# Optimization experiments

Hardware: AMD Instinct MI355X
Metric: run time of the kernel (lower is better)

## Reference

```python
import jax, jax.numpy as jnp
import numpy as np

TARGET_FRAMES = 16
VOXEL_LAMBDA = 20.0
CONF_THRESHOLD = 0.1
CONF_PERCENTILE = 50.0
G = 48  # per-axis voxel grid cap (lambda=20 => ~20-40 occupied cells/axis for randn points)


def setup_inputs() -> dict:
    key = jax.random.key(0)
    k1, k2, k3, k4, k5 = jax.random.split(key, 5)
    B, S, H, W = 1, 128, 224, 224
    return {
        "depth": jax.random.uniform(k1, (B, S, H, W, 1), dtype=jnp.float32),
        "depth_conf": jax.random.uniform(k2, (B, S, H, W), dtype=jnp.float32),
        "world_points": jax.random.normal(k3, (B, S, H, W, 3), dtype=jnp.float32),
        "world_points_conf": jax.random.uniform(k4, (B, S, H, W), dtype=jnp.float32),
        "pose_enc": jax.random.normal(k5, (B, S, 9), dtype=jnp.float32),
    }


def _voxel_occupancy(world_points, world_points_conf):
    # world_points: [1,S,H,W,3], conf: [1,S,H,W]
    pts = world_points[0].reshape(world_points.shape[1], -1, 3)   # [S, HW, 3]
    conf = world_points_conf[0].reshape(world_points.shape[1], -1)  # [S, HW]
    # per-frame confidence filter: conf > thr AND conf >= per-frame percentile
    pct = jnp.quantile(conf, CONF_PERCENTILE / 100.0, axis=1)       # [S]
    valid = (conf > CONF_THRESHOLD) & (conf >= pct[:, None])        # [S, HW]
    big = jnp.float32(1e30)
    pmin = jnp.min(jnp.where(valid[..., None], pts, big), axis=(0, 1))   # [3]
    pmax = jnp.max(jnp.where(valid[..., None], pts, -big), axis=(0, 1))  # [3]
    voxel_size = jnp.min(pmax - pmin) / VOXEL_LAMBDA  # adaptive voxel size
    idx = jnp.floor((pts - pmin) / voxel_size).astype(jnp.int32)
    idx = jnp.clip(idx, 0, G - 1)
    vid = (idx[..., 0] * G + idx[..., 1]) * G + idx[..., 2]  # [S, HW]
    V = G * G * G
    vid = jnp.where(valid, vid, V)  # invalid points -> trash bin V
    S = pts.shape[0]
    occ = jnp.zeros((S, V + 1), dtype=bool).at[jnp.arange(S)[:, None], vid].set(True)
    return occ[:, :V]  # [S, V] per-frame voxel occupancy bitmaps


def _greedy_max_coverage(occ, k):
    S, V = occ.shape

    def step(carry, _):
        covered, selected = carry  # [V] bool, [S] bool
        gains = jnp.sum(occ & ~covered[None, :], axis=1).astype(jnp.float32)  # [S]
        gains = jnp.where(selected, -1.0, gains)
        best = jnp.argmax(gains)  # first max == greedy in-order tie-break
        covered = covered | occ[best]
        selected = selected.at[best].set(True)
        return (covered, selected), (best.astype(jnp.int32), gains[best])

    (covered, _), (sel, scores) = jax.lax.scan(
        step, (jnp.zeros((V,), bool), jnp.zeros((S,), bool)), None, length=k)
    return sel, scores, covered


def reference(depth, depth_conf, world_points, world_points_conf, pose_enc):
    occ = _voxel_occupancy(world_points, world_points_conf)
    sel, scores, covered = _greedy_max_coverage(occ, TARGET_FRAMES)
    total_coverage = jnp.sum(covered).astype(jnp.int32)
    # selected_indices [1,K], coverage_scores [1,K], total_coverage scalar
    return sel[None, :], scores[None, :], total_coverage
```

## Files before the change

### kernel.cpp

```cpp
#include <hip/hip_runtime.h>
#include <hip/hip_bf16.h>
#include <cstdint>

#define S_FRAMES 128
#define HW       50176
#define NGRP     12544
#define GDIM     48
#define VWORDS   3456
#define NBINS    4096
#define CAP      512
#define KSEL     16

#define UWC      512u
#define UCAP_BITS 16384u
#define RQ       9

#define OCCA_OFF  0u
#define OCCB_OFF  (128u*3456u)
#define MM_OFF    (2u*128u*3456u)
#define PCT_OFF   (MM_OFF + 64u*16u)
#define FLAG_OFF  (PCT_OFF + 128u)
#define UW_OFF    (FLAG_OFF + 1u)
#define UNI_OFF   (FLAG_OFF + 16u)
#define CMP_OFF   (UNI_OFF + VWORDS)
#define VB_OFF    (CMP_OFF + 128u*UWC)
#define ZR1_N     1024u
#define ZR2_N     (16u + VWORDS)
#define ZR_TOT    (ZR1_N + ZR2_N)

__device__ __forceinline__ unsigned fkey(float f) {
    unsigned u = __float_as_uint(f);
    return (u & 0x80000000u) ? ~u : (u | 0x80000000u);
}
__device__ __forceinline__ float funkey(unsigned k) {
    unsigned u = (k & 0x80000000u) ? (k & 0x7fffffffu) : ~k;
    return __uint_as_float(u);
}

__global__ __launch_bounds__(1024) void pct_kernel(const float* __restrict__ conf,
                                                   float* __restrict__ pct,
                                                   unsigned* __restrict__ ws) {
    const int s = blockIdx.x;
    const int tid = threadIdx.x;
    const int lane = tid & 63, wid = tid >> 6;
    const float4* c4 = (const float4*)(conf + (size_t)s * HW);

    if (tid < 36) {
        unsigned idx = (unsigned)s * 36u + tid;
        if (idx < ZR_TOT) {
            if (idx < ZR1_N) ws[MM_OFF + idx] = 0u;
            else             ws[FLAG_OFF + (idx - ZR1_N)] = 0u;
        }
    }

    __shared__ unsigned hist[NBINS];
    __shared__ unsigned wtot[16];
    __shared__ unsigned woff[16];
    __shared__ float    list[CAP];
    __shared__ unsigned cnt;
    __shared__ int      rbin[2];
    __shared__ unsigned rcum[2];
    __shared__ float    ab[2];

    for (int b = tid; b < NBINS; b += 1024) hist[b] = 0;
    if (tid == 0) cnt = 0;
    __syncthreads();

    for (int g = tid; g < NGRP; g += 1024) {
        float4 v = c4[g];
        int b0 = min(max((int)(v.x * 4096.0f), 0), NBINS - 1);
        int b1 = min(max((int)(v.y * 4096.0f), 0), NBINS - 1);
        int b2 = min(max((int)(v.z * 4096.0f), 0), NBINS - 1);
        int b3 = min(max((int)(v.w * 4096.0f), 0), NBINS - 1);
        atomicAdd(&hist[b0], 1u); atomicAdd(&hist[b1], 1u);
        atomicAdd(&hist[b2], 1u); atomicAdd(&hist[b3], 1u);
    }
    __syncthreads();

    unsigned chunk = hist[tid * 4] + hist[tid * 4 + 1] + hist[tid * 4 + 2] + hist[tid * 4 + 3];
    unsigned x = chunk;
#pragma unroll
    for (int m = 1; m < 64; m <<= 1) {
        unsigned y = (unsigned)__shfl_up((int)x, m);
        if (lane >= m) x += y;
    }
    if (lane == 63) wtot[wid] = x;
    __syncthreads();
    if (tid < 16) {
        unsigned acc = 0;
        for (int w = 0; w < tid; w++) acc += wtot[w];
        woff[tid] = acc;
    }
    __syncthreads();
    unsigned excl = x - chunk + woff[wid];

    const unsigned R0 = 25087u, R1 = 25088u;
#pragma unroll
    for (int r = 0; r < 2; r++) {
        unsigned rr = r ? R1 : R0;
        if (rr >= excl && rr < excl + chunk) {
            unsigned cum = excl;
            for (int j = 0; j < 4; j++) {
                unsigned h = hist[tid * 4 + j];
                if (rr < cum + h) { rbin[r] = tid * 4 + j; rcum[r] = cum; break; }
                cum += h;
            }
        }
    }
    __syncthreads();

    const int blo = rbin[0], bhi = rbin[1];
    const unsigned cumLo = rcum[0];

    for (int g = tid; g < NGRP; g += 1024) {
        float4 v = c4[g];
        float vv[4] = {v.x, v.y, v.z, v.w};
#pragma unroll
        for (int j = 0; j < 4; j++) {
            int b = min(max((int)(vv[j] * 4096.0f), 0), NBINS - 1);
            if (b >= blo && b <= bhi) {
                unsigned pos = atomicAdd(&cnt, 1u);
                if (pos < CAP) list[pos] = vv[j];
            }
        }
    }
    __syncthreads();

    const int n = (int)min(cnt, (unsigned)CAP);
    const int r0 = (int)(R0 - cumLo), r1 = (int)(R1 - cumLo);
    for (int e = tid; e < n; e += 1024) {
        float xx = list[e];
        int rank = 0;
        for (int j = 0; j < n; j++) {
            float y = list[j];
            rank += (y < xx) || (y == xx && j < e);
        }
        if (rank == r0) ab[0] = xx;
        if (rank == r1) ab[1] = xx;
    }
    __syncthreads();
    if (tid == 0) pct[s] = 0.5f * ab[0] + 0.5f * ab[1];
}

__global__ __launch_bounds__(256) void minmax_kernel(const float* __restrict__ wp,
                                                     const float* __restrict__ conf,
                                                     const float* __restrict__ pct,
                                                     unsigned* __restrict__ ws) {
    const int s = blockIdx.y;
    const int tid = threadIdx.x;
    const int gidx = blockIdx.x * 256 + tid;
    const float pc = pct[s];
    const size_t base = (size_t)s * HW;

    const float4 cf = ((const float4*)(conf + base))[gidx];
    const float4* wp4 = (const float4*)(wp + base * 3) + (size_t)gidx * 3;
    const float4 a = wp4[0], b = wp4[1], d = wp4[2];

    const float BIG = 3.402823466e38f;
    float mnx = BIG, mny = BIG, mnz = BIG;
    float mxx = -BIG, mxy = -BIG, mxz = -BIG;

    float px[4] = {a.x, a.w, b.z, d.y};
    float py[4] = {a.y, b.x, b.w, d.z};
    float pz[4] = {a.z, b.y, d.x, d.w};
    float cc[4] = {cf.x, cf.y, cf.z, cf.w};
    unsigned nib = 0;
#pragma unroll
    for (int j = 0; j < 4; j++) {
        bool v = (cc[j] > 0.1f) && (cc[j] >= pc);
        nib |= (v ? 1u : 0u) << j;
        float x = v ? px[j] : BIG, y = v ? py[j] : BIG, z = v ? pz[j] : BIG;
        mnx = fminf(mnx, x); mny = fminf(mny, y); mnz = fminf(mnz, z);
        x = v ? px[j] : -BIG; y = v ? py[j] : -BIG; z = v ? pz[j] : -BIG;
        mxx = fmaxf(mxx, x); mxy = fmaxf(mxy, y); mxz = fmaxf(mxz, z);
    }

    __shared__ unsigned vbw[32];
    if (tid < 32) vbw[tid] = 0;
    __syncthreads();
    if (nib) atomicOr(&vbw[tid >> 3], nib << ((tid & 7) * 4));

#pragma unroll
    for (int m = 32; m >= 1; m >>= 1) {
        mnx = fminf(mnx, __shfl_xor(mnx, m)); mny = fminf(mny, __shfl_xor(mny, m));
        mnz = fminf(mnz, __shfl_xor(mnz, m));
        mxx = fmaxf(mxx, __shfl_xor(mxx, m)); mxy = fmaxf(mxy, __shfl_xor(mxy, m));
        mxz = fmaxf(mxz, __shfl_xor(mxz, m));
    }
    __shared__ float red[4][6];
    if ((tid & 63) == 0) {
        int w = tid >> 6;
        red[w][0] = mnx; red[w][1] = mny; red[w][2] = mnz;
        red[w][3] = mxx; red[w][4] = mxy; red[w][5] = mxz;
    }
    __syncthreads();
    if (tid < 32)
        ws[VB_OFF + (unsigned)s * 1568u + (unsigned)blockIdx.x * 32u + tid] = vbw[tid];
    if (tid == 0) {
        float r0 = red[0][0], r1 = red[0][1], r2 = red[0][2];
        float r3 = red[0][3], r4 = red[0][4], r5 = red[0][5];
        for (int w = 1; w < 4; w++) {
            r0 = fminf(r0, red[w][0]); r1 = fminf(r1, red[w][1]); r2 = fminf(r2, red[w][2]);
            r3 = fmaxf(r3, red[w][3]); r4 = fmaxf(r4, red[w][4]); r5 = fmaxf(r5, red[w][5]);
        }
        unsigned* slot = ws + MM_OFF + (unsigned)((blockIdx.x + blockIdx.y * 49) & 63) * 16;
        atomicMax(slot + 0, fkey(-r0));
        atomicMax(slot + 1, fkey(-r1));
        atomicMax(slot + 2, fkey(-r2));
        atomicMax(slot + 3, fkey(r3));
        atomicMax(slot + 4, fkey(r4));
        atomicMax(slot + 5, fkey(r5));
    }
}

__global__ __launch_bounds__(512) void voxel_kernel(const float* __restrict__ wp,
                                                    unsigned* __restrict__ ws) {
    const int s = blockIdx.x >> 1;
    const int part = blockIdx.x & 1;
    const int tid = threadIdx.x;

    __shared__ unsigned bm[VWORDS];
    __shared__ float prm[4];
    for (int w = tid; w < VWORDS; w += 512) bm[w] = 0;

    if (tid < 64) {
        const unsigned* sl = ws + MM_OFF + (unsigned)tid * 16;
        unsigned k0 = sl[0], k1 = sl[1], k2 = sl[2], k3 = sl[3], k4 = sl[4], k5 = sl[5];
#pragma unroll
        for (int m = 32; m >= 1; m >>= 1) {
            k0 = max(k0, (unsigned)__shfl_xor((int)k0, m));
            k1 = max(k1, (unsigned)__shfl_xor((int)k1, m));
            k2 = max(k2, (unsigned)__shfl_xor((int)k2, m));
            k3 = max(k3, (unsigned)__shfl_xor((int)k3, m));
            k4 = max(k4, (unsigned)__shfl_xor((int)k4, m));
            k5 = max(k5, (unsigned)__shfl_xor((int)k5, m));
        }
        if (tid == 0) {
            float p0 = -funkey(k0), p1 = -funkey(k1), p2 = -funkey(k2);
            float d0 = funkey(k3) - p0, d1 = funkey(k4) - p1, d2 = funkey(k5) - p2;
            prm[0] = p0; prm[1] = p1; prm[2] = p2;
            prm[3] = fminf(d0, fminf(d1, d2)) / 20.0f;
        }
    }
    __syncthreads();

    const float pmx = prm[0], pmy = prm[1], pmz = prm[2], vs = prm[3];
    const size_t base = (size_t)s * HW;
    const float4* w4 = (const float4*)(wp + base * 3);
    const unsigned* vb = ws + VB_OFF + (unsigned)s * 1568u;

#pragma unroll 1
    for (int k = 0; k < 13; k++) {
        int gl = k * 512 + tid;
        if (gl >= 6272) break;
        int g = part * 6272 + gl;
        unsigned nib = (vb[g >> 3] >> ((g & 7) * 4)) & 0xFu;
        if (!nib) continue;
        const float4* wg = w4 + (size_t)g * 3;
        float4 a = wg[0], b = wg[1], d = wg[2];
        float px[4] = {a.x, a.w, b.z, d.y};
        float py[4] = {a.y, b.x, b.w, d.z};
        float pz[4] = {a.z, b.y, d.x, d.w};
#pragma unroll
        for (int j = 0; j < 4; j++) {
            if ((nib >> j) & 1u) {
                int ix = min(max((int)floorf((px[j] - pmx) / vs), 0), GDIM - 1);
                int iy = min(max((int)floorf((py[j] - pmy) / vs), 0), GDIM - 1);
                int iz = min(max((int)floorf((pz[j] - pmz) / vs), 0), GDIM - 1);
                int vid = (ix * GDIM + iy) * GDIM + iz;
                atomicOr(&bm[vid >> 5], 1u << (vid & 31));
            }
        }
    }
    __syncthreads();

    unsigned* occ = ws + (part ? OCCB_OFF : OCCA_OFF) + (unsigned)s * VWORDS;
    for (int w = tid; w < VWORDS; w += 512) {
        unsigned v = bm[w];
        occ[w] = v;
        if (v) atomicOr(&ws[UNI_OFF + w], v);
    }
}

__global__ __launch_bounds__(1024) void remap_kernel(unsigned* __restrict__ ws) {
    const int f = blockIdx.x;
    const int tid = threadIdx.x;
    const int lane = tid & 63, wid = tid >> 6;

    __shared__ unsigned uni[VWORDS];
    __shared__ unsigned short basew[VWORDS];
    __shared__ unsigned cbm[UWC];
    __shared__ unsigned wtot[16];
    __shared__ unsigned woff[16];
    __shared__ unsigned Ush;

    for (int w = tid; w < VWORDS; w += 1024) uni[w] = ws[UNI_OFF + w];
    for (int w = tid; w < (int)UWC; w += 1024) cbm[w] = 0;
    __syncthreads();

    const int w0 = tid * 4;
    unsigned chunk = 0;
#pragma unroll
    for (int j = 0; j < 4; j++) { int w = w0 + j; if (w < VWORDS) chunk += __popc(uni[w]); }
    unsigned x = chunk;
#pragma unroll
    for (int m = 1; m < 64; m <<= 1) {
        unsigned y = (unsigned)__shfl_up((int)x, m);
        if (lane >= m) x += y;
    }
    if (lane == 63) wtot[wid] = x;
    __syncthreads();
    if (tid < 16) {
        unsigned acc = 0;
        for (int w = 0; w < tid; w++) acc += wtot[w];
        woff[tid] = acc;
    }
    __syncthreads();
    unsigned running = x - chunk + woff[wid];
#pragma unroll
    for (int j = 0; j < 4; j++) {
        int w = w0 + j;
        if (w < VWORDS) { basew[w] = (unsigned short)running; running += __popc(uni[w]); }
    }
    if (tid == 1023) Ush = running;
    __syncthreads();
    const unsigned U = Ush;
    if (f == 0 && tid == 0) { ws[FLAG_OFF] = (U <= UCAP_BITS) ? 2u : 1u; ws[UW_OFF] = (U + 31) >> 5; }
    if (U > UCAP_BITS) return;

    const unsigned* pA = ws + OCCA_OFF + (unsigned)f * VWORDS;
    const unsigned* pB = ws + OCCB_OFF + (unsigned)f * VWORDS;
    for (int w = tid; w < VWORDS; w += 1024) {
        unsigned v = pA[w] | pB[w];
        if (!v) continue;
        unsigned uw = uni[w], b0 = basew[w];
        while (v) {
            int b = __ffs(v) - 1; v &= v - 1;
            unsigned cid = b0 + (unsigned)__popc(uw & ((1u << b) - 1u));
            atomicOr(&cbm[cid >> 5], 1u << (cid & 31));
        }
    }
    __syncthreads();
    for (int w = tid; w < (int)UWC; w += 1024) ws[CMP_OFF + (unsigned)f * UWC + w] = cbm[w];
}

__global__ __launch_bounds__(1024, 1) void greedy1_kernel(unsigned* __restrict__ ws,
                                                          float* __restrict__ out) {
    if (ws[FLAG_OFF] != 2u) return;
    const int tid = threadIdx.x;
    const int f = tid >> 3, sl = tid & 7;
    const unsigned UW = ws[UW_OFF];

    __shared__ unsigned cov[UWC];
    __shared__ int gains[S_FRAMES];
    __shared__ unsigned bestsh;

    for (int w = tid; w < (int)UWC; w += 1024) cov[w] = 0u;
    bool selF = false;
    int best = -1;

    if (UW <= 32u * RQ) {
        uint4 occw[RQ];
        const uint4* my4 = (const uint4*)(ws + CMP_OFF + (unsigned)f * UWC) + sl * RQ;
#pragma unroll
        for (int j = 0; j < RQ; j++) occw[j] = my4[j];
        __syncthreads();

        for (int it = 0; it < KSEL; it++) {
            if (best >= 0 && f == best) {
#pragma unroll
                for (int j = 0; j < RQ; j++) {
                    int w = (sl * RQ + j) * 4;
                    cov[w] |= occw[j].x; cov[w + 1] |= occw[j].y;
                    cov[w + 2] |= occw[j].z; cov[w + 3] |= occw[j].w;
                }
            }
            __syncthreads();
            int g = 0;
#pragma unroll
            for (int j = 0; j < RQ; j++) {
                int w = (sl * RQ + j) * 4;
                g += __popc(occw[j].x & ~cov[w]) + __popc(occw[j].y & ~cov[w + 1])
                   + __popc(occw[j].z & ~cov[w + 2]) + __popc(occw[j].w & ~cov[w + 3]);
            }
            g += __shfl_xor(g, 1); g += __shfl_xor(g, 2); g += __shfl_xor(g, 4);
            if (sl == 0) gains[f] = selF ? -1 : g;
            __syncthreads();
            if (tid < 64) {
                int g1 = gains[tid], g2 = gains[tid + 64];
                unsigned k1 = (g1 < 0) ? 0u : (((unsigned)g1 << 7) | (unsigned)(127 - tid));
                unsigned k2 = (g2 < 0) ? 0u : (((unsigned)g2 << 7) | (unsigned)(63 - tid));
                unsigned k = max(k1, k2);
#pragma unroll
                for (int m = 32; m >= 1; m >>= 1) k = max(k, (unsigned)__shfl_xor((int)k, m));
                if (tid == 0) {
                    bestsh = k;
                    out[it] = (float)(127 - (int)(k & 127u));
                    out[KSEL + it] = (float)(k >> 7);
                }
            }
            __syncthreads();
            best = 127 - (int)(bestsh & 127u);
            if (f == best) selF = true;
        }
        if (f == best) {
#pragma unroll
            for (int j = 0; j < RQ; j++) {
                int w = (sl * RQ + j) * 4;
                cov[w] |= occw[j].x; cov[w + 1] |= occw[j].y;
                cov[w + 2] |= occw[j].z; cov[w + 3] |= occw[j].w;
            }
        }
        __syncthreads();
        if (f == 0) {
            int t = 0;
#pragma unroll
            for (int j = 0; j < RQ; j++) {
                int w = (sl * RQ + j) * 4;
                t += __popc(cov[w]) + __popc(cov[w + 1]) + __popc(cov[w + 2]) + __popc(cov[w + 3]);
            }
            t += __shfl_xor(t, 1); t += __shfl_xor(t, 2); t += __shfl_xor(t, 4);
            if (sl == 0) out[2 * KSEL] = (float)t;
        }
    } else {
        const int Q = (int)((UW + 31) >> 5);
        const uint4* my4 = (const uint4*)(ws + CMP_OFF + (unsigned)f * UWC) + sl * Q;
        __syncthreads();

        for (int it = 0; it < KSEL; it++) {
            if (best >= 0 && f == best) {
                const uint4* b4 = (const uint4*)(ws + CMP_OFF + (unsigned)best * UWC) + sl * Q;
#pragma unroll 4
                for (int j = 0; j < Q; j++) {
                    uint4 o = b4[j];
                    int w = (sl * Q + j) * 4;
                    cov[w] |= o.x; cov[w + 1] |= o.y; cov[w + 2] |= o.z; cov[w + 3] |= o.w;
                }
            }
            __syncthreads();
            int g = 0;
#pragma unroll 4
            for (int j = 0; j < Q; j++) {
                uint4 o = my4[j];
                int w = (sl * Q + j) * 4;
                g += __popc(o.x & ~cov[w]) + __popc(o.y & ~cov[w + 1])
                   + __popc(o.z & ~cov[w + 2]) + __popc(o.w & ~cov[w + 3]);
            }
            g += __shfl_xor(g, 1); g += __shfl_xor(g, 2); g += __shfl_xor(g, 4);
            if (sl == 0) gains[f] = selF ? -1 : g;
            __syncthreads();
            if (tid < 64) {
                int g1 = gains[tid], g2 = gains[tid + 64];
                unsigned k1 = (g1 < 0) ? 0u : (((unsigned)g1 << 7) | (unsigned)(127 - tid));
                unsigned k2 = (g2 < 0) ? 0u : (((unsigned)g2 << 7) | (unsigned)(63 - tid));
                unsigned k = max(k1, k2);
#pragma unroll
                for (int m = 32; m >= 1; m >>= 1) k = max(k, (unsigned)__shfl_xor((int)k, m));
                if (tid == 0) {
                    bestsh = k;
                    out[it] = (float)(127 - (int)(k & 127u));
                    out[KSEL + it] = (float)(k >> 7);
                }
            }
            __syncthreads();
            best = 127 - (int)(bestsh & 127u);
            if (f == best) selF = true;
        }
        if (f == best) {
            const uint4* b4 = (const uint4*)(ws + CMP_OFF + (unsigned)best * UWC) + sl * Q;
#pragma unroll 4
            for (int j = 0; j < Q; j++) {
                uint4 o = b4[j];
                int w = (sl * Q + j) * 4;
                cov[w] |= o.x; cov[w + 1] |= o.y; cov[w + 2] |= o.z; cov[w + 3] |= o.w;
            }
        }
        __syncthreads();
        if (f == 0) {
            int t = 0;
#pragma unroll 4
            for (int j = 0; j < Q; j++) {
                int w = (sl * Q + j) * 4;
                t += __popc(cov[w]) + __popc(cov[w + 1]) + __popc(cov[w + 2]) + __popc(cov[w + 3]);
            }
            t += __shfl_xor(t, 1); t += __shfl_xor(t, 2); t += __shfl_xor(t, 4);
            if (sl == 0) out[2 * KSEL] = (float)t;
        }
    }
}

extern "C" void kernel_launch(void* const* d_in, const int* in_sizes, int n_in,
                              void* d_out, int out_size, void* d_ws, size_t ws_size,
                              hipStream_t stream) {
    const float* wp   = (const float*)d_in[2];
    const float* conf = (const float*)d_in[3];
    float* out = (float*)d_out;
    unsigned* ws = (unsigned*)d_ws;

    float* pct = (float*)(ws + PCT_OFF);
    pct_kernel<<<128, 1024, 0, stream>>>(conf, pct, ws);
    minmax_kernel<<<dim3(49, 128), 256, 0, stream>>>(wp, conf, pct, ws);
    voxel_kernel<<<256, 512, 0, stream>>>(wp, ws);
    remap_kernel<<<128, 1024, 0, stream>>>(ws);
    greedy1_kernel<<<1, 1024, 0, stream>>>(ws, out);
}
```

Before: 229.0 us.

## Fuse percentile with min/max pass and greedy into remap via last-block counter

Merges the percentile and min/max kernels, so each frame's block computes its median and then scans only valid points for bounds and validity bits. It stores per-frame min/max directly instead of using atomic sortable keys. The greedy selection now runs in the last remap block, chosen through an atomic ticket counter, which cuts launches from five to three. The trade-off is much less parallelism in the min/max pass (128 blocks instead of 6272) and a threadfence-based handoff between blocks.

```diff
diff --git a/kernel.cpp b/kernel.cpp
--- a/kernel.cpp
+++ b/kernel.cpp
@@ -10,6 +10,7 @@
 #define NBINS    4096
 #define CAP      512
 #define KSEL     16
+#define VBW      1568
 
 #define UWC      512u
 #define UCAP_BITS 16384u
@@ -18,42 +19,24 @@
 #define OCCA_OFF  0u
 #define OCCB_OFF  (128u*3456u)
 #define MM_OFF    (2u*128u*3456u)
-#define PCT_OFF   (MM_OFF + 64u*16u)
-#define FLAG_OFF  (PCT_OFF + 128u)
-#define UW_OFF    (FLAG_OFF + 1u)
-#define UNI_OFF   (FLAG_OFF + 16u)
+#define CTR_OFF   (MM_OFF + 1024u)
+#define UNI_OFF   (CTR_OFF + 16u)
 #define CMP_OFF   (UNI_OFF + VWORDS)
 #define VB_OFF    (CMP_OFF + 128u*UWC)
-#define ZR1_N     1024u
-#define ZR2_N     (16u + VWORDS)
-#define ZR_TOT    (ZR1_N + ZR2_N)
-
-__device__ __forceinline__ unsigned fkey(float f) {
-    unsigned u = __float_as_uint(f);
-    return (u & 0x80000000u) ? ~u : (u | 0x80000000u);
-}
-__device__ __forceinline__ float funkey(unsigned k) {
-    unsigned u = (k & 0x80000000u) ? (k & 0x7fffffffu) : ~k;
-    return __uint_as_float(u);
-}
-
-__global__ __launch_bounds__(1024) void pct_kernel(const float* __restrict__ conf,
-                                                   float* __restrict__ pct,
-                                                   unsigned* __restrict__ ws) {
+
+__global__ __launch_bounds__(1024) void fused_stats_kernel(const float* __restrict__ conf,
+                                                           const float* __restrict__ wp,
+                                                           unsigned* __restrict__ ws) {
     const int s = blockIdx.x;
     const int tid = threadIdx.x;
     const int lane = tid & 63, wid = tid >> 6;
     const float4* c4 = (const float4*)(conf + (size_t)s * HW);
 
-    if (tid < 36) {
-        unsigned idx = (unsigned)s * 36u + tid;
-        if (idx < ZR_TOT) {
-            if (idx < ZR1_N) ws[MM_OFF + idx] = 0u;
-            else             ws[FLAG_OFF + (idx - ZR1_N)] = 0u;
-        }
-    }
+    if (tid < 27) ws[UNI_OFF + (unsigned)s * 27u + tid] = 0u;
+    if (s == 0 && tid == 31) ws[CTR_OFF] = 0u;
 
     __shared__ unsigned hist[NBINS];
+    __shared__ unsigned vbw[VBW];
     __shared__ unsigned wtot[16];
     __shared__ unsigned woff[16];
     __shared__ float    list[CAP];
@@ -61,8 +44,11 @@
     __shared__ int      rbin[2];
     __shared__ unsigned rcum[2];
     __shared__ float    ab[2];
+    __shared__ float    medsh;
+    __shared__ float    red[16][6];
 
     for (int b = tid; b < NBINS; b += 1024) hist[b] = 0;
+    for (int w = tid; w < VBW; w += 1024) vbw[w] = 0;
     if (tid == 0) cnt = 0;
     __syncthreads();
 
@@ -139,46 +125,41 @@
         if (rank == r1) ab[1] = xx;
     }
     __syncthreads();
-    if (tid == 0) pct[s] = 0.5f * ab[0] + 0.5f * ab[1];
-}
-
-__global__ __launch_bounds__(256) void minmax_kernel(const float* __restrict__ wp,
-                                                     const float* __restrict__ conf,
-                                                     const float* __restrict__ pct,
-                                                     unsigned* __restrict__ ws) {
-    const int s = blockIdx.y;
-    const int tid = threadIdx.x;
-    const int gidx = blockIdx.x * 256 + tid;
-    const float pc = pct[s];
+    if (tid == 0) medsh = 0.5f * ab[0] + 0.5f * ab[1];
+    __syncthreads();
+    const float med = medsh;
+
     const size_t base = (size_t)s * HW;
-
-    const float4 cf = ((const float4*)(conf + base))[gidx];
-    const float4* wp4 = (const float4*)(wp + base * 3) + (size_t)gidx * 3;
-    const float4 a = wp4[0], b = wp4[1], d = wp4[2];
-
+    const float4* wp4 = (const float4*)(wp + base * 3);
     const float BIG = 3.402823466e38f;
     float mnx = BIG, mny = BIG, mnz = BIG;
     float mxx = -BIG, mxy = -BIG, mxz = -BIG;
 
-    float px[4] = {a.x, a.w, b.z, d.y};
-    float py[4] = {a.y, b.x, b.w, d.z};
-    float pz[4] = {a.z, b.y, d.x, d.w};
-    float cc[4] = {cf.x, cf.y, cf.z, cf.w};
-    unsigned nib = 0;
-#pragma unroll
-    for (int j = 0; j < 4; j++) {
-        bool v = (cc[j] > 0.1f) && (cc[j] >= pc);
-        nib |= (v ? 1u : 0u) << j;
-        float x = v ? px[j] : BIG, y = v ? py[j] : BIG, z = v ? pz[j] : BIG;
-        mnx = fminf(mnx, x); mny = fminf(mny, y); mnz = fminf(mnz, z);
-        x = v ? px[j] : -BIG; y = v ? py[j] : -BIG; z = v ? pz[j] : -BIG;
-        mxx = fmaxf(mxx, x); mxy = fmaxf(mxy, y); mxz = fmaxf(mxz, z);
-    }
-
-    __shared__ unsigned vbw[32];
-    if (tid < 32) vbw[tid] = 0;
-    __syncthreads();
-    if (nib) atomicOr(&vbw[tid >> 3], nib << ((tid & 7) * 4));
+    for (int g = tid; g < NGRP; g += 1024) {
+        float4 v = c4[g];
+        float cc[4] = {v.x, v.y, v.z, v.w};
+        unsigned nib = 0;
+#pragma unroll
+        for (int j = 0; j < 4; j++) {
+            bool val = (cc[j] > 0.1f) && (cc[j] >= med);
+            nib |= (val ? 1u : 0u) << j;
+        }
+        if (nib) {
+            atomicOr(&vbw[g >> 3], nib << ((g & 7) * 4));
+            const float4* wg = wp4 + (size_t)g * 3;
+            float4 a = wg[0], bb = wg[1], d = wg[2];
+            float px[4] = {a.x, a.w, bb.z, d.y};
+            float py[4] = {a.y, bb.x, bb.w, d.z};
+            float pz[4] = {a.z, bb.y, d.x, d.w};
+#pragma unroll
+            for (int j = 0; j < 4; j++) {
+                if ((nib >> j) & 1u) {
+                    mnx = fminf(mnx, px[j]); mny = fminf(mny, py[j]); mnz = fminf(mnz, pz[j]);
+                    mxx = fmaxf(mxx, px[j]); mxy = fmaxf(mxy, py[j]); mxz = fmaxf(mxz, pz[j]);
+                }
+            }
+        }
+    }
 
 #pragma unroll
     for (int m = 32; m >= 1; m >>= 1) {
@@ -187,59 +168,50 @@
         mxx = fmaxf(mxx, __shfl_xor(mxx, m)); mxy = fmaxf(mxy, __shfl_xor(mxy, m));
         mxz = fmaxf(mxz, __shfl_xor(mxz, m));
     }
-    __shared__ float red[4][6];
-    if ((tid & 63) == 0) {
-        int w = tid >> 6;
-        red[w][0] = mnx; red[w][1] = mny; red[w][2] = mnz;
-        red[w][3] = mxx; red[w][4] = mxy; red[w][5] = mxz;
-    }
-    __syncthreads();
-    if (tid < 32)
-        ws[VB_OFF + (unsigned)s * 1568u + (unsigned)blockIdx.x * 32u + tid] = vbw[tid];
+    if (lane == 0) {
+        red[wid][0] = mnx; red[wid][1] = mny; red[wid][2] = mnz;
+        red[wid][3] = mxx; red[wid][4] = mxy; red[wid][5] = mxz;
+    }
+    __syncthreads();
     if (tid == 0) {
-        float r0 = red[0][0], r1 = red[0][1], r2 = red[0][2];
-        float r3 = red[0][3], r4 = red[0][4], r5 = red[0][5];
-        for (int w = 1; w < 4; w++) {
-            r0 = fminf(r0, red[w][0]); r1 = fminf(r1, red[w][1]); r2 = fminf(r2, red[w][2]);
-            r3 = fmaxf(r3, red[w][3]); r4 = fmaxf(r4, red[w][4]); r5 = fmaxf(r5, red[w][5]);
-        }
-        unsigned* slot = ws + MM_OFF + (unsigned)((blockIdx.x + blockIdx.y * 49) & 63) * 16;
-        atomicMax(slot + 0, fkey(-r0));
-        atomicMax(slot + 1, fkey(-r1));
-        atomicMax(slot + 2, fkey(-r2));
-        atomicMax(slot + 3, fkey(r3));
-        atomicMax(slot + 4, fkey(r4));
-        atomicMax(slot + 5, fkey(r5));
-    }
+        float r0f = red[0][0], r1f = red[0][1], r2f = red[0][2];
+        float r3f = red[0][3], r4f = red[0][4], r5f = red[0][5];
+        for (int w = 1; w < 16; w++) {
+            r0f = fminf(r0f, red[w][0]); r1f = fminf(r1f, red[w][1]); r2f = fminf(r2f, red[w][2]);
+            r3f = fmaxf(r3f, red[w][3]); r4f = fmaxf(r4f, red[w][4]); r5f = fmaxf(r5f, red[w][5]);
+        }
+        float* slot = (float*)(ws + MM_OFF) + (size_t)s * 8;
+        slot[0] = r0f; slot[1] = r1f; slot[2] = r2f;
+        slot[3] = r3f; slot[4] = r4f; slot[5] = r5f;
+    }
+    for (int w = tid; w < VBW; w += 1024) ws[VB_OFF + (unsigned)s * 1568u + w] = vbw[w];
 }
 
-__global__ __launch_bounds__(512) void voxel_kernel(const float* __restrict__ wp,
-                                                    unsigned* __restrict__ ws) {
+__global__ __launch_bounds__(1024) void voxel_kernel(const float* __restrict__ wp,
+                                                     unsigned* __restrict__ ws) {
     const int s = blockIdx.x >> 1;
     const int part = blockIdx.x & 1;
     const int tid = threadIdx.x;
 
     __shared__ unsigned bm[VWORDS];
     __shared__ float prm[4];
-    for (int w = tid; w < VWORDS; w += 512) bm[w] = 0;
+    for (int w = tid; w < VWORDS; w += 1024) bm[w] = 0;
 
     if (tid < 64) {
-        const unsigned* sl = ws + MM_OFF + (unsigned)tid * 16;
-        unsigned k0 = sl[0], k1 = sl[1], k2 = sl[2], k3 = sl[3], k4 = sl[4], k5 = sl[5];
+        const float* m0 = (const float*)(ws + MM_OFF) + (size_t)tid * 8;
+        const float* m1 = m0 + 64 * 8;
+        float mnx = fminf(m0[0], m1[0]), mny = fminf(m0[1], m1[1]), mnz = fminf(m0[2], m1[2]);
+        float mxx = fmaxf(m0[3], m1[3]), mxy = fmaxf(m0[4], m1[4]), mxz = fmaxf(m0[5], m1[5]);
 #pragma unroll
         for (int m = 32; m >= 1; m >>= 1) {
-            k0 = max(k0, (unsigned)__shfl_xor((int)k0, m));
-            k1 = max(k1, (unsigned)__shfl_xor((int)k1, m));
-            k2 = max(k2, (unsigned)__shfl_xor((int)k2, m));
-            k3 = max(k3, (unsigned)__shfl_xor((int)k3, m));
-            k4 = max(k4, (unsigned)__shfl_xor((int)k4, m));
-            k5 = max(k5, (unsigned)__shfl_xor((int)k5, m));
+            mnx = fminf(mnx, __shfl_xor(mnx, m)); mny = fminf(mny, __shfl_xor(mny, m));
+            mnz = fminf(mnz, __shfl_xor(mnz, m));
+            mxx = fmaxf(mxx, __shfl_xor(mxx, m)); mxy = fmaxf(mxy, __shfl_xor(mxy, m));
+            mxz = fmaxf(mxz, __shfl_xor(mxz, m));
         }
         if (tid == 0) {
-            float p0 = -funkey(k0), p1 = -funkey(k1), p2 = -funkey(k2);
-            float d0 = funkey(k3) - p0, d1 = funkey(k4) - p1, d2 = funkey(k5) - p2;
-            prm[0] = p0; prm[1] = p1; prm[2] = p2;
-            prm[3] = fminf(d0, fminf(d1, d2)) / 20.0f;
+            prm[0] = mnx; prm[1] = mny; prm[2] = mnz;
+            prm[3] = fminf(mxx - mnx, fminf(mxy - mny, mxz - mnz)) / 20.0f;
         }
     }
     __syncthreads();
@@ -250,8 +222,8 @@
     const unsigned* vb = ws + VB_OFF + (unsigned)s * 1568u;
 
 #pragma unroll 1
-    for (int k = 0; k < 13; k++) {
-        int gl = k * 512 + tid;
+    for (int k = 0; k < 7; k++) {
+        int gl = k * 1024 + tid;
         if (gl >= 6272) break;
         int g = part * 6272 + gl;
         unsigned nib = (vb[g >> 3] >> ((g & 7) * 4)) & 0xFu;
@@ -275,14 +247,15 @@
     __syncthreads();
 
     unsigned* occ = ws + (part ? OCCB_OFF : OCCA_OFF) + (unsigned)s * VWORDS;
-    for (int w = tid; w < VWORDS; w += 512) {
+    for (int w = tid; w < VWORDS; w += 1024) {
         unsigned v = bm[w];
         occ[w] = v;
         if (v) atomicOr(&ws[UNI_OFF + w], v);
     }
 }
 
-__global__ __launch_bounds__(1024) void remap_kernel(unsigned* __restrict__ ws) {
+__global__ __launch_bounds__(1024, 1) void remap_greedy_kernel(unsigned* __restrict__ ws,
+                                                               float* __restrict__ out) {
     const int f = blockIdx.x;
     const int tid = threadIdx.x;
     const int lane = tid & 63, wid = tid >> 6;
@@ -293,6 +266,10 @@
     __shared__ unsigned wtot[16];
     __shared__ unsigned woff[16];
     __shared__ unsigned Ush;
+    __shared__ unsigned rank_sh;
+    __shared__ unsigned cov[UWC];
+    __shared__ int gains[S_FRAMES];
+    __shared__ unsigned bestsh;
 
     for (int w = tid; w < VWORDS; w += 1024) uni[w] = ws[UNI_OFF + w];
     for (int w = tid; w < (int)UWC; w += 1024) cbm[w] = 0;
@@ -325,7 +302,6 @@
     if (tid == 1023) Ush = running;
     __syncthreads();
     const unsigned U = Ush;
-    if (f == 0 && tid == 0) { ws[FLAG_OFF] = (U <= UCAP_BITS) ? 2u : 1u; ws[UW_OFF] = (U + 31) >> 5; }
     if (U > UCAP_BITS) return;
 
     const unsigned* pA = ws + OCCA_OFF + (unsigned)f * VWORDS;
@@ -342,18 +318,18 @@
     }
     __syncthreads();
     for (int w = tid; w < (int)UWC; w += 1024) ws[CMP_OFF + (unsigned)f * UWC + w] = cbm[w];
-}
-
-__global__ __launch_bounds__(1024, 1) void greedy1_kernel(unsigned* __restrict__ ws,
-                                                          float* __restrict__ out) {
-    if (ws[FLAG_OFF] != 2u) return;
-    const int tid = threadIdx.x;
-    const int f = tid >> 3, sl = tid & 7;
-    const unsigned UW = ws[UW_OFF];
-
-    __shared__ unsigned cov[UWC];
-    __shared__ int gains[S_FRAMES];
-    __shared__ unsigned bestsh;
+
+    __syncthreads();
+    if (tid == 0) {
+        __threadfence();
+        rank_sh = atomicAdd(&ws[CTR_OFF], 1u);
+    }
+    __syncthreads();
+    if (rank_sh != (unsigned)(S_FRAMES - 1)) return;
+    __threadfence();
+
+    const int gf = tid >> 3, sl = tid & 7;
+    const unsigned UW = (U + 31u) >> 5;
 
     for (int w = tid; w < (int)UWC; w += 1024) cov[w] = 0u;
     bool selF = false;
@@ -361,13 +337,13 @@
 
     if (UW <= 32u * RQ) {
         uint4 occw[RQ];
-        const uint4* my4 = (const uint4*)(ws + CMP_OFF + (unsigned)f * UWC) + sl * RQ;
+        const uint4* my4 = (const uint4*)(ws + CMP_OFF + (unsigned)gf * UWC) + sl * RQ;
 #pragma unroll
         for (int j = 0; j < RQ; j++) occw[j] = my4[j];
         __syncthreads();
 
         for (int it = 0; it < KSEL; it++) {
-            if (best >= 0 && f == best) {
+            if (best >= 0 && gf == best) {
 #pragma unroll
                 for (int j = 0; j < RQ; j++) {
                     int w = (sl * RQ + j) * 4;
@@ -384,7 +360,7 @@
                    + __popc(occw[j].z & ~cov[w + 2]) + __popc(occw[j].w & ~cov[w + 3]);
             }
             g += __shfl_xor(g, 1); g += __shfl_xor(g, 2); g += __shfl_xor(g, 4);
-            if (sl == 0) gains[f] = selF ? -1 : g;
+            if (sl == 0) gains[gf] = selF ? -1 : g;
             __syncthreads();
             if (tid < 64) {
                 int g1 = gains[tid], g2 = gains[tid + 64];
@@ -401,9 +377,9 @@
             }
             __syncthreads();
             best = 127 - (int)(bestsh & 127u);
-            if (f == best) selF = true;
-        }
-        if (f == best) {
+            if (gf == best) selF = true;
+        }
+        if (gf == best) {
 #pragma unroll
             for (int j = 0; j < RQ; j++) {
                 int w = (sl * RQ + j) * 4;
@@ -412,7 +388,7 @@
             }
         }
         __syncthreads();
-        if (f == 0) {
+        if (gf == 0) {
             int t = 0;
 #pragma unroll
             for (int j = 0; j < RQ; j++) {
@@ -424,11 +400,11 @@
         }
     } else {
         const int Q = (int)((UW + 31) >> 5);
-        const uint4* my4 = (const uint4*)(ws + CMP_OFF + (unsigned)f * UWC) + sl * Q;
+        const uint4* my4 = (const uint4*)(ws + CMP_OFF + (unsigned)gf * UWC) + sl * Q;
         __syncthreads();
 
         for (int it = 0; it < KSEL; it++) {
-            if (best >= 0 && f == best) {
+            if (best >= 0 && gf == best) {
                 const uint4* b4 = (const uint4*)(ws + CMP_OFF + (unsigned)best * UWC) + sl * Q;
 #pragma unroll 4
                 for (int j = 0; j < Q; j++) {
@@ -447,7 +423,7 @@
                    + __popc(o.z & ~cov[w + 2]) + __popc(o.w & ~cov[w + 3]);
             }
             g += __shfl_xor(g, 1); g += __shfl_xor(g, 2); g += __shfl_xor(g, 4);
-            if (sl == 0) gains[f] = selF ? -1 : g;
+            if (sl == 0) gains[gf] = selF ? -1 : g;
             __syncthreads();
             if (tid < 64) {
                 int g1 = gains[tid], g2 = gains[tid + 64];
@@ -464,9 +440,9 @@
             }
             __syncthreads();
             best = 127 - (int)(bestsh & 127u);
-            if (f == best) selF = true;
-        }
-        if (f == best) {
+            if (gf == best) selF = true;
+        }
+        if (gf == best) {
             const uint4* b4 = (const uint4*)(ws + CMP_OFF + (unsigned)best * UWC) + sl * Q;
 #pragma unroll 4
             for (int j = 0; j < Q; j++) {
@@ -476,7 +452,7 @@
             }
         }
         __syncthreads();
-        if (f == 0) {
+        if (gf == 0) {
             int t = 0;
 #pragma unroll 4
             for (int j = 0; j < Q; j++) {
@@ -497,10 +473,7 @@
     float* out = (float*)d_out;
     unsigned* ws = (unsigned*)d_ws;
 
-    float* pct = (float*)(ws + PCT_OFF);
-    pct_kernel<<<128, 1024, 0, stream>>>(conf, pct, ws);
-    minmax_kernel<<<dim3(49, 128), 256, 0, stream>>>(wp, conf, pct, ws);
-    voxel_kernel<<<256, 512, 0, stream>>>(wp, ws);
-    remap_kernel<<<128, 1024, 0, stream>>>(ws);
-    greedy1_kernel<<<1, 1024, 0, stream>>>(ws, out);
+    fused_stats_kernel<<<128, 1024, 0, stream>>>(conf, wp, ws);
+    voxel_kernel<<<256, 1024, 0, stream>>>(wp, ws);
+    remap_greedy_kernel<<<128, 1024, 0, stream>>>(ws, out);
 }
```

Result: slower. 235.4 us (+2.8%).

## Split histogram across two blocks per frame and fuse remap with greedy via last-block

Applied to the files above, without the earlier changes.

Each frame's confidence histogram is now built by two blocks that merge into a global histogram, and whichever block arrives last computes the median. Remap and greedy selection are merged into one kernel, with the last finishing block running the greedy step, which removes a launch and the flag handshake. The voxel kernel moves to 1024 threads and issues its point loads before the validity check. Workspace zeroing moves to a hipMemsetAsync that now also clears the 128x4096 global histogram, adding memory traffic and an extra stream op.

```diff
diff --git a/kernel.cpp b/kernel.cpp
--- a/kernel.cpp
+++ b/kernel.cpp
@@ -5,11 +5,13 @@
 #define S_FRAMES 128
 #define HW       50176
 #define NGRP     12544
+#define HALFG    6272
 #define GDIM     48
 #define VWORDS   3456
 #define NBINS    4096
 #define CAP      512
 #define KSEL     16
+#define VBW      1568
 
 #define UWC      512u
 #define UCAP_BITS 16384u
@@ -18,15 +20,14 @@
 #define OCCA_OFF  0u
 #define OCCB_OFF  (128u*3456u)
 #define MM_OFF    (2u*128u*3456u)
-#define PCT_OFF   (MM_OFF + 64u*16u)
-#define FLAG_OFF  (PCT_OFF + 128u)
-#define UW_OFF    (FLAG_OFF + 1u)
-#define UNI_OFF   (FLAG_OFF + 16u)
-#define CMP_OFF   (UNI_OFF + VWORDS)
+#define CTR_OFF   (MM_OFF + 1024u)
+#define HCTR_OFF  (CTR_OFF + 16u)
+#define UNI_OFF   (HCTR_OFF + 128u)
+#define HIST_OFF  (UNI_OFF + VWORDS)
+#define ZERO_WORDS (1024u + 16u + 128u + VWORDS + 128u*4096u)
+#define PCT_OFF   (HIST_OFF + 128u*4096u)
+#define CMP_OFF   (PCT_OFF + 128u)
 #define VB_OFF    (CMP_OFF + 128u*UWC)
-#define ZR1_N     1024u
-#define ZR2_N     (16u + VWORDS)
-#define ZR_TOT    (ZR1_N + ZR2_N)
 
 __device__ __forceinline__ unsigned fkey(float f) {
     unsigned u = __float_as_uint(f);
@@ -37,21 +38,14 @@
     return __uint_as_float(u);
 }
 
-__global__ __launch_bounds__(1024) void pct_kernel(const float* __restrict__ conf,
-                                                   float* __restrict__ pct,
-                                                   unsigned* __restrict__ ws) {
-    const int s = blockIdx.x;
+__global__ __launch_bounds__(1024) void hist_median_kernel(const float* __restrict__ conf,
+                                                           float* __restrict__ pct,
+                                                           unsigned* __restrict__ ws) {
+    const int s = blockIdx.x >> 1;
+    const int half = blockIdx.x & 1;
     const int tid = threadIdx.x;
     const int lane = tid & 63, wid = tid >> 6;
     const float4* c4 = (const float4*)(conf + (size_t)s * HW);
-
-    if (tid < 36) {
-        unsigned idx = (unsigned)s * 36u + tid;
-        if (idx < ZR_TOT) {
-            if (idx < ZR1_N) ws[MM_OFF + idx] = 0u;
-            else             ws[FLAG_OFF + (idx - ZR1_N)] = 0u;
-        }
-    }
 
     __shared__ unsigned hist[NBINS];
     __shared__ unsigned wtot[16];
@@ -61,13 +55,14 @@
     __shared__ int      rbin[2];
     __shared__ unsigned rcum[2];
     __shared__ float    ab[2];
+    __shared__ unsigned rank_sh;
 
     for (int b = tid; b < NBINS; b += 1024) hist[b] = 0;
-    if (tid == 0) cnt = 0;
-    __syncthreads();
-
-    for (int g = tid; g < NGRP; g += 1024) {
-        float4 v = c4[g];
+    __syncthreads();
+
+    const int g0 = half * HALFG;
+    for (int gl = tid; gl < HALFG; gl += 1024) {
+        float4 v = c4[g0 + gl];
         int b0 = min(max((int)(v.x * 4096.0f), 0), NBINS - 1);
         int b1 = min(max((int)(v.y * 4096.0f), 0), NBINS - 1);
         int b2 = min(max((int)(v.z * 4096.0f), 0), NBINS - 1);
@@ -75,6 +70,25 @@
         atomicAdd(&hist[b0], 1u); atomicAdd(&hist[b1], 1u);
         atomicAdd(&hist[b2], 1u); atomicAdd(&hist[b3], 1u);
     }
+    __syncthreads();
+
+    unsigned* gh = ws + HIST_OFF + (unsigned)s * NBINS;
+#pragma unroll
+    for (int j = 0; j < 4; j++) {
+        unsigned h = hist[tid + j * 1024];
+        if (h) atomicAdd(&gh[tid + j * 1024], h);
+    }
+    __syncthreads();
+    if (tid == 0) {
+        __threadfence();
+        rank_sh = atomicAdd(&ws[HCTR_OFF + s], 1u);
+    }
+    __syncthreads();
+    if (rank_sh != 1u) return;
+    __threadfence();
+
+    for (int b = tid; b < NBINS; b += 1024) hist[b] = gh[b];
+    if (tid == 0) cnt = 0;
     __syncthreads();
 
     unsigned chunk = hist[tid * 4] + hist[tid * 4 + 1] + hist[tid * 4 + 2] + hist[tid * 4 + 3];
@@ -213,15 +227,15 @@
     }
 }
 
-__global__ __launch_bounds__(512) void voxel_kernel(const float* __restrict__ wp,
-                                                    unsigned* __restrict__ ws) {
+__global__ __launch_bounds__(1024) void voxel_kernel(const float* __restrict__ wp,
+                                                     unsigned* __restrict__ ws) {
     const int s = blockIdx.x >> 1;
     const int part = blockIdx.x & 1;
     const int tid = threadIdx.x;
 
     __shared__ unsigned bm[VWORDS];
     __shared__ float prm[4];
-    for (int w = tid; w < VWORDS; w += 512) bm[w] = 0;
+    for (int w = tid; w < VWORDS; w += 1024) bm[w] = 0;
 
     if (tid < 64) {
         const unsigned* sl = ws + MM_OFF + (unsigned)tid * 16;
@@ -250,39 +264,41 @@
     const unsigned* vb = ws + VB_OFF + (unsigned)s * 1568u;
 
 #pragma unroll 1
-    for (int k = 0; k < 13; k++) {
-        int gl = k * 512 + tid;
-        if (gl >= 6272) break;
-        int g = part * 6272 + gl;
-        unsigned nib = (vb[g >> 3] >> ((g & 7) * 4)) & 0xFu;
-        if (!nib) continue;
+    for (int k = 0; k < 7; k++) {
+        int gl = k * 1024 + tid;
+        if (gl >= HALFG) break;
+        int g = part * HALFG + gl;
         const float4* wg = w4 + (size_t)g * 3;
         float4 a = wg[0], b = wg[1], d = wg[2];
-        float px[4] = {a.x, a.w, b.z, d.y};
-        float py[4] = {a.y, b.x, b.w, d.z};
-        float pz[4] = {a.z, b.y, d.x, d.w};
-#pragma unroll
-        for (int j = 0; j < 4; j++) {
-            if ((nib >> j) & 1u) {
-                int ix = min(max((int)floorf((px[j] - pmx) / vs), 0), GDIM - 1);
-                int iy = min(max((int)floorf((py[j] - pmy) / vs), 0), GDIM - 1);
-                int iz = min(max((int)floorf((pz[j] - pmz) / vs), 0), GDIM - 1);
-                int vid = (ix * GDIM + iy) * GDIM + iz;
-                atomicOr(&bm[vid >> 5], 1u << (vid & 31));
+        unsigned nib = (vb[g >> 3] >> ((g & 7) * 4)) & 0xFu;
+        if (nib) {
+            float px[4] = {a.x, a.w, b.z, d.y};
+            float py[4] = {a.y, b.x, b.w, d.z};
+            float pz[4] = {a.z, b.y, d.x, d.w};
+#pragma unroll
+            for (int j = 0; j < 4; j++) {
+                if ((nib >> j) & 1u) {
+                    int ix = min(max((int)floorf((px[j] - pmx) / vs), 0), GDIM - 1);
+                    int iy = min(max((int)floorf((py[j] - pmy) / vs), 0), GDIM - 1);
+                    int iz = min(max((int)floorf((pz[j] - pmz) / vs), 0), GDIM - 1);
+                    int vid = (ix * GDIM + iy) * GDIM + iz;
+                    atomicOr(&bm[vid >> 5], 1u << (vid & 31));
+                }
             }
         }
     }
     __syncthreads();
 
     unsigned* occ = ws + (part ? OCCB_OFF : OCCA_OFF) + (unsigned)s * VWORDS;
-    for (int w = tid; w < VWORDS; w += 512) {
+    for (int w = tid; w < VWORDS; w += 1024) {
         unsigned v = bm[w];
         occ[w] = v;
         if (v) atomicOr(&ws[UNI_OFF + w], v);
     }
 }
 
-__global__ __launch_bounds__(1024) void remap_kernel(unsigned* __restrict__ ws) {
+__global__ __launch_bounds__(1024, 1) void remap_greedy_kernel(unsigned* __restrict__ ws,
+                                                               float* __restrict__ out) {
     const int f = blockIdx.x;
     const int tid = threadIdx.x;
     const int lane = tid & 63, wid = tid >> 6;
@@ -293,6 +309,10 @@
     __shared__ unsigned wtot[16];
     __shared__ unsigned woff[16];
     __shared__ unsigned Ush;
+    __shared__ unsigned rank_sh;
+    __shared__ unsigned cov[UWC];
+    __shared__ int gains[S_FRAMES];
+    __shared__ unsigned bestsh;
 
     for (int w = tid; w < VWORDS; w += 1024) uni[w] = ws[UNI_OFF + w];
     for (int w = tid; w < (int)UWC; w += 1024) cbm[w] = 0;
@@ -325,7 +345,6 @@
     if (tid == 1023) Ush = running;
     __syncthreads();
     const unsigned U = Ush;
-    if (f == 0 && tid == 0) { ws[FLAG_OFF] = (U <= UCAP_BITS) ? 2u : 1u; ws[UW_OFF] = (U + 31) >> 5; }
     if (U > UCAP_BITS) return;
 
     const unsigned* pA = ws + OCCA_OFF + (unsigned)f * VWORDS;
@@ -342,18 +361,18 @@
     }
     __syncthreads();
     for (int w = tid; w < (int)UWC; w += 1024) ws[CMP_OFF + (unsigned)f * UWC + w] = cbm[w];
-}
-
-__global__ __launch_bounds__(1024, 1) void greedy1_kernel(unsigned* __restrict__ ws,
-                                                          float* __restrict__ out) {
-    if (ws[FLAG_OFF] != 2u) return;
-    const int tid = threadIdx.x;
-    const int f = tid >> 3, sl = tid & 7;
-    const unsigned UW = ws[UW_OFF];
-
-    __shared__ unsigned cov[UWC];
-    __shared__ int gains[S_FRAMES];
-    __shared__ unsigned bestsh;
+
+    __syncthreads();
+    if (tid == 0) {
+        __threadfence();
+        rank_sh = atomicAdd(&ws[CTR_OFF], 1u);
+    }
+    __syncthreads();
+    if (rank_sh != (unsigned)(S_FRAMES - 1)) return;
+    __threadfence();
+
+    const int gf = tid >> 3, sl = tid & 7;
+    const unsigned UW = (U + 31u) >> 5;
 
     for (int w = tid; w < (int)UWC; w += 1024) cov[w] = 0u;
     bool selF = false;
@@ -361,13 +380,13 @@
 
     if (UW <= 32u * RQ) {
         uint4 occw[RQ];
-        const uint4* my4 = (const uint4*)(ws + CMP_OFF + (unsigned)f * UWC) + sl * RQ;
+        const uint4* my4 = (const uint4*)(ws + CMP_OFF + (unsigned)gf * UWC) + sl * RQ;
 #pragma unroll
         for (int j = 0; j < RQ; j++) occw[j] = my4[j];
         __syncthreads();
 
         for (int it = 0; it < KSEL; it++) {
-            if (best >= 0 && f == best) {
+            if (best >= 0 && gf == best) {
 #pragma unroll
                 for (int j = 0; j < RQ; j++) {
                     int w = (sl * RQ + j) * 4;
@@ -384,7 +403,7 @@
                    + __popc(occw[j].z & ~cov[w + 2]) + __popc(occw[j].w & ~cov[w + 3]);
             }
             g += __shfl_xor(g, 1); g += __shfl_xor(g, 2); g += __shfl_xor(g, 4);
-            if (sl == 0) gains[f] = selF ? -1 : g;
+            if (sl == 0) gains[gf] = selF ? -1 : g;
             __syncthreads();
             if (tid < 64) {
                 int g1 = gains[tid], g2 = gains[tid + 64];
@@ -401,9 +420,9 @@
             }
             __syncthreads();
             best = 127 - (int)(bestsh & 127u);
-            if (f == best) selF = true;
-        }
-        if (f == best) {
+            if (gf == best) selF = true;
+        }
+        if (gf == best) {
 #pragma unroll
             for (int j = 0; j < RQ; j++) {
                 int w = (sl * RQ + j) * 4;
@@ -412,7 +431,7 @@
             }
         }
         __syncthreads();
-        if (f == 0) {
+        if (gf == 0) {
             int t = 0;
 #pragma unroll
             for (int j = 0; j < RQ; j++) {
@@ -424,11 +443,11 @@
         }
     } else {
         const int Q = (int)((UW + 31) >> 5);
-        const uint4* my4 = (const uint4*)(ws + CMP_OFF + (unsigned)f * UWC) + sl * Q;
+        const uint4* my4 = (const uint4*)(ws + CMP_OFF + (unsigned)gf * UWC) + sl * Q;
         __syncthreads();
 
         for (int it = 0; it < KSEL; it++) {
-            if (best >= 0 && f == best) {
+            if (best >= 0 && gf == best) {
                 const uint4* b4 = (const uint4*)(ws + CMP_OFF + (unsigned)best * UWC) + sl * Q;
 #pragma unroll 4
                 for (int j = 0; j < Q; j++) {
@@ -447,7 +466,7 @@
                    + __popc(o.z & ~cov[w + 2]) + __popc(o.w & ~cov[w + 3]);
             }
             g += __shfl_xor(g, 1); g += __shfl_xor(g, 2); g += __shfl_xor(g, 4);
-            if (sl == 0) gains[f] = selF ? -1 : g;
+            if (sl == 0) gains[gf] = selF ? -1 : g;
             __syncthreads();
             if (tid < 64) {
                 int g1 = gains[tid], g2 = gains[tid + 64];
@@ -464,9 +483,9 @@
             }
             __syncthreads();
             best = 127 - (int)(bestsh & 127u);
-            if (f == best) selF = true;
-        }
-        if (f == best) {
+            if (gf == best) selF = true;
+        }
+        if (gf == best) {
             const uint4* b4 = (const uint4*)(ws + CMP_OFF + (unsigned)best * UWC) + sl * Q;
 #pragma unroll 4
             for (int j = 0; j < Q; j++) {
@@ -476,7 +495,7 @@
             }
         }
         __syncthreads();
-        if (f == 0) {
+        if (gf == 0) {
             int t = 0;
 #pragma unroll 4
             for (int j = 0; j < Q; j++) {
@@ -496,11 +515,12 @@
     const float* conf = (const float*)d_in[3];
     float* out = (float*)d_out;
     unsigned* ws = (unsigned*)d_ws;
-
     float* pct = (float*)(ws + PCT_OFF);
-    pct_kernel<<<128, 1024, 0, stream>>>(conf, pct, ws);
+
+    hipMemsetAsync(ws + MM_OFF, 0, (size_t)ZERO_WORDS * 4, stream);
+
+    hist_median_kernel<<<256, 1024, 0, stream>>>(conf, pct, ws);
     minmax_kernel<<<dim3(49, 128), 256, 0, stream>>>(wp, conf, pct, ws);
-    voxel_kernel<<<256, 512, 0, stream>>>(wp, ws);
-    remap_kernel<<<128, 1024, 0, stream>>>(ws);
-    greedy1_kernel<<<1, 1024, 0, stream>>>(ws, out);
-}
+    voxel_kernel<<<256, 1024, 0, stream>>>(wp, ws);
+    remap_greedy_kernel<<<128, 1024, 0, stream>>>(ws, out);
+}
```

Result: slower. 290.5 us (+26.8%).

## Split remap per half-frame with atomic merge, widen voxel blocks, memset workspace

Applied to the files above, without the earlier changes.

Zeroing of workspace moves out of pct_kernel into a hipMemsetAsync that also clears the compact bitmap region, so remap blocks can merge with atomicOr. The remap kernel now runs two blocks per frame, one per occupancy half, instead of one block OR-ing both halves. The voxel kernel goes from 512 to 1024 threads per block, and its point loads are issued before the validity nibble check. The aim is more parallelism in remap and voxel, at the cost of an extra memset launch, duplicated prefix-scan work per remap block, and global atomics.

```diff
diff --git a/kernel.cpp b/kernel.cpp
--- a/kernel.cpp
+++ b/kernel.cpp
@@ -5,11 +5,13 @@
 #define S_FRAMES 128
 #define HW       50176
 #define NGRP     12544
+#define HALFG    6272
 #define GDIM     48
 #define VWORDS   3456
 #define NBINS    4096
 #define CAP      512
 #define KSEL     16
+#define VBW      1568
 
 #define UWC      512u
 #define UCAP_BITS 16384u
@@ -18,15 +20,13 @@
 #define OCCA_OFF  0u
 #define OCCB_OFF  (128u*3456u)
 #define MM_OFF    (2u*128u*3456u)
-#define PCT_OFF   (MM_OFF + 64u*16u)
-#define FLAG_OFF  (PCT_OFF + 128u)
+#define FLAG_OFF  (MM_OFF + 1024u)
 #define UW_OFF    (FLAG_OFF + 1u)
 #define UNI_OFF   (FLAG_OFF + 16u)
-#define CMP_OFF   (UNI_OFF + VWORDS)
+#define PCT_OFF   (UNI_OFF + VWORDS)
+#define CMP_OFF   (PCT_OFF + 128u)
 #define VB_OFF    (CMP_OFF + 128u*UWC)
-#define ZR1_N     1024u
-#define ZR2_N     (16u + VWORDS)
-#define ZR_TOT    (ZR1_N + ZR2_N)
+#define ZERO_WORDS (1024u + 16u + (unsigned)VWORDS + 128u + 128u*UWC)
 
 __device__ __forceinline__ unsigned fkey(float f) {
     unsigned u = __float_as_uint(f);
@@ -38,20 +38,11 @@
 }
 
 __global__ __launch_bounds__(1024) void pct_kernel(const float* __restrict__ conf,
-                                                   float* __restrict__ pct,
-                                                   unsigned* __restrict__ ws) {
+                                                   float* __restrict__ pct) {
     const int s = blockIdx.x;
     const int tid = threadIdx.x;
     const int lane = tid & 63, wid = tid >> 6;
     const float4* c4 = (const float4*)(conf + (size_t)s * HW);
-
-    if (tid < 36) {
-        unsigned idx = (unsigned)s * 36u + tid;
-        if (idx < ZR_TOT) {
-            if (idx < ZR1_N) ws[MM_OFF + idx] = 0u;
-            else             ws[FLAG_OFF + (idx - ZR1_N)] = 0u;
-        }
-    }
 
     __shared__ unsigned hist[NBINS];
     __shared__ unsigned wtot[16];
@@ -213,15 +204,15 @@
     }
 }
 
-__global__ __launch_bounds__(512) void voxel_kernel(const float* __restrict__ wp,
-                                                    unsigned* __restrict__ ws) {
+__global__ __launch_bounds__(1024) void voxel_kernel(const float* __restrict__ wp,
+                                                     unsigned* __restrict__ ws) {
     const int s = blockIdx.x >> 1;
     const int part = blockIdx.x & 1;
     const int tid = threadIdx.x;
 
     __shared__ unsigned bm[VWORDS];
     __shared__ float prm[4];
-    for (int w = tid; w < VWORDS; w += 512) bm[w] = 0;
+    for (int w = tid; w < VWORDS; w += 1024) bm[w] = 0;
 
     if (tid < 64) {
         const unsigned* sl = ws + MM_OFF + (unsigned)tid * 16;
@@ -250,32 +241,33 @@
     const unsigned* vb = ws + VB_OFF + (unsigned)s * 1568u;
 
 #pragma unroll 1
-    for (int k = 0; k < 13; k++) {
-        int gl = k * 512 + tid;
-        if (gl >= 6272) break;
-        int g = part * 6272 + gl;
-        unsigned nib = (vb[g >> 3] >> ((g & 7) * 4)) & 0xFu;
-        if (!nib) continue;
+    for (int k = 0; k < 7; k++) {
+        int gl = k * 1024 + tid;
+        if (gl >= HALFG) break;
+        int g = part * HALFG + gl;
         const float4* wg = w4 + (size_t)g * 3;
         float4 a = wg[0], b = wg[1], d = wg[2];
-        float px[4] = {a.x, a.w, b.z, d.y};
-        float py[4] = {a.y, b.x, b.w, d.z};
-        float pz[4] = {a.z, b.y, d.x, d.w};
-#pragma unroll
-        for (int j = 0; j < 4; j++) {
-            if ((nib >> j) & 1u) {
-                int ix = min(max((int)floorf((px[j] - pmx) / vs), 0), GDIM - 1);
-                int iy = min(max((int)floorf((py[j] - pmy) / vs), 0), GDIM - 1);
-                int iz = min(max((int)floorf((pz[j] - pmz) / vs), 0), GDIM - 1);
-                int vid = (ix * GDIM + iy) * GDIM + iz;
-                atomicOr(&bm[vid >> 5], 1u << (vid & 31));
+        unsigned nib = (vb[g >> 3] >> ((g & 7) * 4)) & 0xFu;
+        if (nib) {
+            float px[4] = {a.x, a.w, b.z, d.y};
+            float py[4] = {a.y, b.x, b.w, d.z};
+            float pz[4] = {a.z, b.y, d.x, d.w};
+#pragma unroll
+            for (int j = 0; j < 4; j++) {
+                if ((nib >> j) & 1u) {
+                    int ix = min(max((int)floorf((px[j] - pmx) / vs), 0), GDIM - 1);
+                    int iy = min(max((int)floorf((py[j] - pmy) / vs), 0), GDIM - 1);
+                    int iz = min(max((int)floorf((pz[j] - pmz) / vs), 0), GDIM - 1);
+                    int vid = (ix * GDIM + iy) * GDIM + iz;
+                    atomicOr(&bm[vid >> 5], 1u << (vid & 31));
+                }
             }
         }
     }
     __syncthreads();
 
     unsigned* occ = ws + (part ? OCCB_OFF : OCCA_OFF) + (unsigned)s * VWORDS;
-    for (int w = tid; w < VWORDS; w += 512) {
+    for (int w = tid; w < VWORDS; w += 1024) {
         unsigned v = bm[w];
         occ[w] = v;
         if (v) atomicOr(&ws[UNI_OFF + w], v);
@@ -283,7 +275,8 @@
 }
 
 __global__ __launch_bounds__(1024) void remap_kernel(unsigned* __restrict__ ws) {
-    const int f = blockIdx.x;
+    const int f = blockIdx.x >> 1;
+    const int part = blockIdx.x & 1;
     const int tid = threadIdx.x;
     const int lane = tid & 63, wid = tid >> 6;
 
@@ -325,13 +318,15 @@
     if (tid == 1023) Ush = running;
     __syncthreads();
     const unsigned U = Ush;
-    if (f == 0 && tid == 0) { ws[FLAG_OFF] = (U <= UCAP_BITS) ? 2u : 1u; ws[UW_OFF] = (U + 31) >> 5; }
+    if (blockIdx.x == 0 && tid == 0) {
+        ws[FLAG_OFF] = (U <= UCAP_BITS) ? 2u : 1u;
+        ws[UW_OFF] = (U + 31) >> 5;
+    }
     if (U > UCAP_BITS) return;
 
-    const unsigned* pA = ws + OCCA_OFF + (unsigned)f * VWORDS;
-    const unsigned* pB = ws + OCCB_OFF + (unsigned)f * VWORDS;
+    const unsigned* pl = ws + (part ? OCCB_OFF : OCCA_OFF) + (unsigned)f * VWORDS;
     for (int w = tid; w < VWORDS; w += 1024) {
-        unsigned v = pA[w] | pB[w];
+        unsigned v = pl[w];
         if (!v) continue;
         unsigned uw = uni[w], b0 = basew[w];
         while (v) {
@@ -341,7 +336,10 @@
         }
     }
     __syncthreads();
-    for (int w = tid; w < (int)UWC; w += 1024) ws[CMP_OFF + (unsigned)f * UWC + w] = cbm[w];
+    for (int w = tid; w < (int)UWC; w += 1024) {
+        unsigned v = cbm[w];
+        if (v) atomicOr(&ws[CMP_OFF + (unsigned)f * UWC + w], v);
+    }
 }
 
 __global__ __launch_bounds__(1024, 1) void greedy1_kernel(unsigned* __restrict__ ws,
@@ -496,11 +494,13 @@
     const float* conf = (const float*)d_in[3];
     float* out = (float*)d_out;
     unsigned* ws = (unsigned*)d_ws;
-
     float* pct = (float*)(ws + PCT_OFF);
-    pct_kernel<<<128, 1024, 0, stream>>>(conf, pct, ws);
+
+    hipMemsetAsync(ws + MM_OFF, 0, (size_t)ZERO_WORDS * 4, stream);
+
+    pct_kernel<<<128, 1024, 0, stream>>>(conf, pct);
     minmax_kernel<<<dim3(49, 128), 256, 0, stream>>>(wp, conf, pct, ws);
-    voxel_kernel<<<256, 512, 0, stream>>>(wp, ws);
-    remap_kernel<<<128, 1024, 0, stream>>>(ws);
+    voxel_kernel<<<256, 1024, 0, stream>>>(wp, ws);
+    remap_kernel<<<256, 1024, 0, stream>>>(ws);
     greedy1_kernel<<<1, 1024, 0, stream>>>(ws, out);
 }
```

Result: no change. 228.1 us (-0.4%).
